# Optimization experiments

Hardware: AMD Instinct MI355X
Metric: run time of the kernel (lower is better)

Reference implementation:

```python
import jax, jax.numpy as jnp
import numpy as np
from jax import lax

N, D, H = 4096, 256, 4


def setup_inputs() -> dict:
    key = jax.random.key(0)
    ks = jax.random.split(key, 6)
    x = jax.random.normal(ks[0], (1, 1, N, D), dtype=jnp.float32)
    adj = jax.random.randint(ks[1], (N, N), 0, 2, dtype=jnp.int32)
    conv_w = jax.random.normal(ks[2], (1, 1, 1, 1), dtype=jnp.float32)
    conv_b = jax.random.normal(ks[3], (1,), dtype=jnp.float32)
    # xavier_uniform on (H, 2D, 1) with gain 1.414
    limit = 1.414 * np.sqrt(6.0 / (2 * D + 1))
    a = jax.random.uniform(ks[4], (H, 2 * D, 1), minval=-limit, maxval=limit, dtype=jnp.float32)
    bias = jnp.zeros((D,), dtype=jnp.float32)
    return {"x": x, "adj": adj, "conv_w": conv_w, "conv_b": conv_b, "a": a, "bias": bias}


def reference(x, adj, conv_w, conv_b, a, bias):
    # 1x1 conv (NCHW / OIHW), preserves spatial dims
    h = lax.conv_general_dilated(x, conv_w, (1, 1), 'VALID',
                                 dimension_numbers=('NCHW', 'OIHW', 'NCHW'))
    h = h + conv_b[None, :, None, None]
    h = h[0, 0]                      # [N, D]
    d = h.shape[1]
    a1 = a[:, :d, 0]                 # [H, D]
    a2 = a[:, d:, 0]                 # [H, D]
    Wh1 = h @ a1.T                   # [N, H]
    Wh2 = h @ a2.T                   # [N, H]
    # e[k, i, j] = elu(Wh1[i, k] + Wh2[j, k])
    e = jax.nn.elu(Wh1.T[:, :, None] + Wh2.T[:, None, :])   # [H, N, N]
    att = jnp.where((adj > 0)[None, :, :], e, jnp.float32(-9e15))
    att = jax.nn.softmax(att, axis=-1)
    # dropout is inactive in eval mode (self.training=False)
    h_pass = jnp.einsum('hij,jd->hid', att, h).mean(axis=0)  # [N, D]
    out = jax.nn.elu(0.5 * h_pass + 0.5 * h)
    norm = jnp.maximum(jnp.linalg.norm(out, axis=1, keepdims=True), 1e-12)
    out = out / norm
    return out + bias
```

## Files before the change

### kernel.cpp

```cpp
#include <hip/hip_runtime.h>
#include <math.h>

#define NN 4096
#define DD 256
#define HH 4
#define SPLIT 8
#define BKG 64

typedef short short8 __attribute__((ext_vector_type(8)));
typedef float float4v __attribute__((ext_vector_type(4)));

__device__ __forceinline__ unsigned short f2bf(float f) {
  unsigned u = __float_as_uint(f);
  u += 0x7FFF + ((u >> 16) & 1);
  return (unsigned short)(u >> 16);
}
__device__ __forceinline__ unsigned f2bf_pk(float a, float b) {
  unsigned ua = __float_as_uint(a); ua += 0x7FFF + ((ua >> 16) & 1);
  unsigned ub = __float_as_uint(b); ub += 0x7FFF + ((ub >> 16) & 1);
  return __builtin_amdgcn_perm(ub, ua, 0x07060302);
}
__device__ __forceinline__ void gld16(void* lds, const void* gp) {
  __builtin_amdgcn_global_load_lds(
      (const __attribute__((address_space(1))) unsigned int*)gp,
      (__attribute__((address_space(3))) unsigned int*)lds, 16, 0, 0);
}

__global__ void k_zero(float* __restrict__ hp) {
  int idx = blockIdx.x * 256 + threadIdx.x;
  ((float4*)hp)[idx] = make_float4(0.f, 0.f, 0.f, 0.f);
}

__global__ __launch_bounds__(256) void k_pre(
    const float* __restrict__ x, const float* __restrict__ a,
    const float* __restrict__ cwp, const float* __restrict__ cbp,
    unsigned short* __restrict__ hbfT, float* __restrict__ Rpg,
    unsigned short* __restrict__ Ebf) {
  const int tid = threadIdx.x;
  const int bid = blockIdx.x;
  const float cw = cwp[0], cb = cbp[0];

  if (bid < 256) {
    __shared__ float t[64][65];
    const int j0 = (bid & 63) * 64, d0 = (bid >> 6) * 64;
    const int r = tid >> 4, c4 = tid & 15;
#pragma unroll
    for (int p = 0; p < 4; p++) {
      const int jj = p * 16 + r;
      const float4 v = *(const float4*)(x + (size_t)(j0 + jj) * DD + d0 + c4 * 4);
      t[jj][c4 * 4 + 0] = v.x * cw + cb;
      t[jj][c4 * 4 + 1] = v.y * cw + cb;
      t[jj][c4 * 4 + 2] = v.z * cw + cb;
      t[jj][c4 * 4 + 3] = v.w * cw + cb;
    }
    __syncthreads();
    const int jc = (tid & 15) * 4, db = tid >> 4;
#pragma unroll
    for (int p = 0; p < 4; p++) {
      const int dd = p * 16 + db;
      const unsigned l0 = f2bf(t[jc + 0][dd]);
      const unsigned l1 = f2bf(t[jc + 1][dd]);
      const unsigned l2 = f2bf(t[jc + 2][dd]);
      const unsigned l3 = f2bf(t[jc + 3][dd]);
      uint2 val;
      val.x = l0 | (l1 << 16);
      val.y = l2 | (l3 << 16);
      *(uint2*)(hbfT + (size_t)(d0 + dd) * NN + j0 + jc) = val;
    }
  } else {
    const int ln = tid >> 2, qd = (tid & 3) * 64;
    const int node = (bid - 256) * 64 + ln;
    float p1[HH] = {0.f, 0.f, 0.f, 0.f}, p2[HH] = {0.f, 0.f, 0.f, 0.f};
#pragma unroll
    for (int k = 0; k < 16; k++) {
      const int d = qd + k * 4;
      const float4 v = *(const float4*)(x + (size_t)node * DD + d);
      const float h0 = v.x * cw + cb, h1 = v.y * cw + cb;
      const float h2 = v.z * cw + cb, h3 = v.w * cw + cb;
#pragma unroll
      for (int h = 0; h < HH; h++) {
        const float4 a1 = *(const float4*)(a + h * 512 + d);
        const float4 a2 = *(const float4*)(a + h * 512 + 256 + d);
        p1[h] += h0 * a1.x + h1 * a1.y + h2 * a1.z + h3 * a1.w;
        p2[h] += h0 * a2.x + h1 * a2.y + h2 * a2.z + h3 * a2.w;
      }
    }
#pragma unroll
    for (int off = 1; off <= 2; off <<= 1) {
#pragma unroll
      for (int h = 0; h < HH; h++) {
        p1[h] += __shfl_xor(p1[h], off);
        p2[h] += __shfl_xor(p2[h], off);
      }
    }
    if ((tid & 3) == 0) {
#pragma unroll
      for (int h = 0; h < HH; h++) {
        Rpg[h * NN + node] = __expf(p1[h]);
        Ebf[h * NN + node] = f2bf(__expf(p2[h]));
      }
    }
  }
}

__global__ __launch_bounds__(256) void k_zw(
    const int* __restrict__ adj, const float* __restrict__ Rpg,
    const unsigned short* __restrict__ Ebf, unsigned short* __restrict__ Wm) {
  __shared__ float red[4][HH];
  __shared__ float sZi[HH];

  const int i = blockIdx.x;
  const int tid = threadIdx.x;
  const float C = 0.36787944117144233f;
  float Rp[HH], z[HH];
#pragma unroll
  for (int h = 0; h < HH; h++) {
    Rp[h] = Rpg[h * NN + i];
    z[h] = 0.f;
  }
  unsigned P[4][HH][2];
  const int4* arow = (const int4*)(adj + (size_t)i * NN);
#pragma unroll
  for (int k = 0; k < 4; k++) {
    const int j4 = tid + k * 256;
    const int4 av = arow[j4];
    const bool m0 = av.x > 0, m1 = av.y > 0, m2 = av.z > 0, m3 = av.w > 0;
#pragma unroll
    for (int h = 0; h < HH; h++) {
      const uint2 e2 = *(const uint2*)(Ebf + (size_t)h * NN + j4 * 4);
      const float E0 = __uint_as_float(e2.x << 16);
      const float E1 = __uint_as_float(e2.x & 0xffff0000u);
      const float E2 = __uint_as_float(e2.y << 16);
      const float E3 = __uint_as_float(e2.y & 0xffff0000u);
      float u, p0, p1, p2, p3;
      u = Rp[h] * E0; p0 = u > 1.f ? u : C * __expf(u); p0 = m0 ? p0 : 0.f;
      u = Rp[h] * E1; p1 = u > 1.f ? u : C * __expf(u); p1 = m1 ? p1 : 0.f;
      u = Rp[h] * E2; p2 = u > 1.f ? u : C * __expf(u); p2 = m2 ? p2 : 0.f;
      u = Rp[h] * E3; p3 = u > 1.f ? u : C * __expf(u); p3 = m3 ? p3 : 0.f;
      z[h] += (p0 + p1) + (p2 + p3);
      P[k][h][0] = f2bf_pk(p0, p1);
      P[k][h][1] = f2bf_pk(p2, p3);
    }
  }
#pragma unroll
  for (int h = 0; h < HH; h++) {
#pragma unroll
    for (int off = 32; off; off >>= 1) z[h] += __shfl_xor(z[h], off);
  }
  const int lane = tid & 63, wv = tid >> 6;
  if (lane == 0) {
#pragma unroll
    for (int h = 0; h < HH; h++) red[wv][h] = z[h];
  }
  __syncthreads();
  if (tid < HH) {
    const float zt = red[0][tid] + red[1][tid] + red[2][tid] + red[3][tid];
    sZi[tid] = zt > 0.f ? 0.25f / zt : 0.f;
  }
  __syncthreads();
  float Zi[HH];
#pragma unroll
  for (int h = 0; h < HH; h++) Zi[h] = sZi[h];

  unsigned* wrow = (unsigned*)(Wm + (size_t)i * NN);
#pragma unroll
  for (int k = 0; k < 4; k++) {
    const int j4 = tid + k * 256;
    float w0 = 0.f, w1 = 0.f, w2 = 0.f, w3 = 0.f;
#pragma unroll
    for (int h = 0; h < HH; h++) {
      const unsigned pa = P[k][h][0];
      const unsigned pb = P[k][h][1];
      w0 += __uint_as_float(pa << 16) * Zi[h];
      w1 += __uint_as_float(pa & 0xffff0000u) * Zi[h];
      w2 += __uint_as_float(pb << 16) * Zi[h];
      w3 += __uint_as_float(pb & 0xffff0000u) * Zi[h];
    }
    wrow[j4 * 2] = f2bf_pk(w0, w1);
    wrow[j4 * 2 + 1] = f2bf_pk(w2, w3);
  }
}

__global__ __launch_bounds__(256) void k_gemm(
    const unsigned short* __restrict__ Wm, const unsigned short* __restrict__ hbfT,
    float* __restrict__ hpOut, int useSplit) {
  __shared__ __align__(16) unsigned short sA[64 * 64];
  __shared__ __align__(16) unsigned short sB[256 * 64];
  const int tid = threadIdx.x;
  const int wv = tid >> 6, lane = tid & 63;
  const int m16 = lane & 15, q = lane >> 4, m7 = m16 & 7;
  const int rb = blockIdx.x >> 3, sp = blockIdx.x & 7;
  const int i0 = rb * 64;
  const int jlo = sp * (NN / SPLIT);
  const int lr = lane >> 3;
  const int lk8 = (lane & 7) ^ lr;

  float4v acc[4][4];
#pragma unroll
  for (int a = 0; a < 4; a++)
#pragma unroll
    for (int b = 0; b < 4; b++) acc[a][b] = (float4v)0.f;

  for (int kt = 0; kt < (NN / SPLIT) / BKG; kt++) {
    const int j0 = jlo + kt * BKG;
    __syncthreads();
#pragma unroll
    for (int t = 0; t < 2; t++) {
      const int r0 = wv * 16 + t * 8;
      gld16(sA + r0 * 64, Wm + (size_t)(i0 + r0 + lr) * NN + j0 + lk8 * 8);
    }
#pragma unroll
    for (int t = 0; t < 8; t++) {
      const int r0 = wv * 64 + t * 8;
      gld16(sB + r0 * 64, hbfT + (size_t)(r0 + lr) * NN + j0 + lk8 * 8);
    }
    __syncthreads();
#pragma unroll
    for (int ks = 0; ks < 2; ks++) {
      const int kp = ((ks * 4 + q) ^ m7) * 8;
      short8 aF[4], bF[4];
#pragma unroll
      for (int it = 0; it < 4; it++)
        aF[it] = *(const short8*)(sA + (it * 16 + m16) * 64 + kp);
#pragma unroll
      for (int dt = 0; dt < 4; dt++)
        bF[dt] = *(const short8*)(sB + (wv * 64 + dt * 16 + m16) * 64 + kp);
#pragma unroll
      for (int it = 0; it < 4; it++)
#pragma unroll
        for (int dt = 0; dt < 4; dt++)
          acc[it][dt] = __builtin_amdgcn_mfma_f32_16x16x32_bf16(aF[it], bF[dt], acc[it][dt], 0, 0, 0);
    }
  }

  if (useSplit) {
    float* base = hpOut + (size_t)sp * NN * DD;
#pragma unroll
    for (int it = 0; it < 4; it++)
#pragma unroll
      for (int dt = 0; dt < 4; dt++) {
        const int d = wv * 64 + dt * 16 + m16;
#pragma unroll
        for (int rg = 0; rg < 4; rg++)
          base[(size_t)(i0 + it * 16 + q * 4 + rg) * DD + d] = acc[it][dt][rg];
      }
  } else {
#pragma unroll
    for (int it = 0; it < 4; it++)
#pragma unroll
      for (int dt = 0; dt < 4; dt++) {
        const int d = wv * 64 + dt * 16 + m16;
#pragma unroll
        for (int rg = 0; rg < 4; rg++)
          atomicAdd(&hpOut[(size_t)(i0 + it * 16 + q * 4 + rg) * DD + d], acc[it][dt][rg]);
      }
  }
}

__global__ __launch_bounds__(256) void k_epi(
    const float* __restrict__ hp, int nsplit, const float* __restrict__ x,
    const float* __restrict__ cwp, const float* __restrict__ cbp,
    const float* __restrict__ bias, float* __restrict__ out) {
  const int lane = threadIdx.x & 63, wv = threadIdx.x >> 6;
  const int i = blockIdx.x * 4 + wv;
  const float cw = cwp[0], cb = cbp[0];
  const int d4 = lane * 4;
  float4 pv = make_float4(0.f, 0.f, 0.f, 0.f);
  for (int s = 0; s < nsplit; s++) {
    const float4 t = *(const float4*)(hp + (size_t)s * NN * DD + (size_t)i * DD + d4);
    pv.x += t.x; pv.y += t.y; pv.z += t.z; pv.w += t.w;
  }
  const float4 xv = *(const float4*)(x + (size_t)i * DD + d4);
  float4 v;
  v.x = 0.5f * pv.x + 0.5f * (xv.x * cw + cb);
  v.y = 0.5f * pv.y + 0.5f * (xv.y * cw + cb);
  v.z = 0.5f * pv.z + 0.5f * (xv.z * cw + cb);
  v.w = 0.5f * pv.w + 0.5f * (xv.w * cw + cb);
  v.x = v.x > 0.f ? v.x : expm1f(v.x);
  v.y = v.y > 0.f ? v.y : expm1f(v.y);
  v.z = v.z > 0.f ? v.z : expm1f(v.z);
  v.w = v.w > 0.f ? v.w : expm1f(v.w);
  float ss = v.x * v.x + v.y * v.y + v.z * v.z + v.w * v.w;
#pragma unroll
  for (int off = 32; off; off >>= 1) ss += __shfl_xor(ss, off);
  const float inv = 1.f / fmaxf(sqrtf(ss), 1e-12f);
  const float4 bv = *(const float4*)(bias + d4);
  float4 o;
  o.x = v.x * inv + bv.x;
  o.y = v.y * inv + bv.y;
  o.z = v.z * inv + bv.z;
  o.w = v.w * inv + bv.w;
  *(float4*)(out + (size_t)i * DD + d4) = o;
}

extern "C" void kernel_launch(void* const* d_in, const int* in_sizes, int n_in,
                              void* d_out, int out_size, void* d_ws, size_t ws_size,
                              hipStream_t stream) {
  const float* x = (const float*)d_in[0];
  const int* adj = (const int*)d_in[1];
  const float* cw = (const float*)d_in[2];
  const float* cb = (const float*)d_in[3];
  const float* a = (const float*)d_in[4];
  const float* bias = (const float*)d_in[5];
  float* out = (float*)d_out;
  float* ws = (float*)d_ws;

  float* Rpg = ws;
  unsigned short* Ebf = (unsigned short*)(ws + 16384);
  unsigned short* hbfT = (unsigned short*)(ws + 24576);
  unsigned short* Wm = (unsigned short*)(ws + 24576 + 524288);
  float* hp = ws + 24576 + 524288 + 8388608;

  const size_t needSplit =
      (size_t)(24576 + 524288 + 8388608 + (size_t)SPLIT * NN * DD) * 4;
  const int useSplit = (ws_size >= needSplit) ? 1 : 0;
  const int nsplit = useSplit ? SPLIT : 1;

  if (!useSplit) hipLaunchKernelGGL(k_zero, dim3(1024), dim3(256), 0, stream, hp);
  hipLaunchKernelGGL(k_pre, dim3(320), dim3(256), 0, stream, x, a, cw, cb, hbfT, Rpg, Ebf);
  hipLaunchKernelGGL(k_zw, dim3(NN), dim3(256), 0, stream, adj, Rpg, Ebf, Wm);
  hipLaunchKernelGGL(k_gemm, dim3(64 * SPLIT), dim3(256), 0, stream, Wm, hbfT, hp, useSplit);
  hipLaunchKernelGGL(k_epi, dim3(1024), dim3(256), 0, stream, hp, nsplit, x, cw, cb, bias, out);
}
```

Before: 165.5 us.

## Double-buffer GEMM LDS tiles and keep attention probabilities in fp32 registers

The GEMM kernel now uses two dynamic shared-memory buffers and issues the global-to-LDS loads for the next K tile before computing on the current one. This removes one barrier per iteration and overlaps load latency with the MFMA work. In exchange, LDS use doubles to 80KB, which can lower occupancy. Separately, k_zw keeps the per-head probabilities as fp32 instead of packing them to bf16. This drops the pack and unpack ALU work and rounding, at the cost of more registers.

```diff
diff --git a/kernel.cpp b/kernel.cpp
--- a/kernel.cpp
+++ b/kernel.cpp
@@ -118,7 +118,7 @@
     Rp[h] = Rpg[h * NN + i];
     z[h] = 0.f;
   }
-  unsigned P[4][HH][2];
+  float P[4][HH][4];
   const int4* arow = (const int4*)(adj + (size_t)i * NN);
 #pragma unroll
   for (int k = 0; k < 4; k++) {
@@ -138,8 +138,7 @@
       u = Rp[h] * E2; p2 = u > 1.f ? u : C * __expf(u); p2 = m2 ? p2 : 0.f;
       u = Rp[h] * E3; p3 = u > 1.f ? u : C * __expf(u); p3 = m3 ? p3 : 0.f;
       z[h] += (p0 + p1) + (p2 + p3);
-      P[k][h][0] = f2bf_pk(p0, p1);
-      P[k][h][1] = f2bf_pk(p2, p3);
+      P[k][h][0] = p0; P[k][h][1] = p1; P[k][h][2] = p2; P[k][h][3] = p3;
     }
   }
 #pragma unroll
@@ -169,12 +168,10 @@
     float w0 = 0.f, w1 = 0.f, w2 = 0.f, w3 = 0.f;
 #pragma unroll
     for (int h = 0; h < HH; h++) {
-      const unsigned pa = P[k][h][0];
-      const unsigned pb = P[k][h][1];
-      w0 += __uint_as_float(pa << 16) * Zi[h];
-      w1 += __uint_as_float(pa & 0xffff0000u) * Zi[h];
-      w2 += __uint_as_float(pb << 16) * Zi[h];
-      w3 += __uint_as_float(pb & 0xffff0000u) * Zi[h];
+      w0 += P[k][h][0] * Zi[h];
+      w1 += P[k][h][1] * Zi[h];
+      w2 += P[k][h][2] * Zi[h];
+      w3 += P[k][h][3] * Zi[h];
     }
     wrow[j4 * 2] = f2bf_pk(w0, w1);
     wrow[j4 * 2 + 1] = f2bf_pk(w2, w3);
@@ -184,8 +181,11 @@
 __global__ __launch_bounds__(256) void k_gemm(
     const unsigned short* __restrict__ Wm, const unsigned short* __restrict__ hbfT,
     float* __restrict__ hpOut, int useSplit) {
-  __shared__ __align__(16) unsigned short sA[64 * 64];
-  __shared__ __align__(16) unsigned short sB[256 * 64];
+  extern __shared__ __align__(16) unsigned short smem[];
+  unsigned short* sA0 = smem;
+  unsigned short* sA1 = smem + 4096;
+  unsigned short* sB0 = smem + 8192;
+  unsigned short* sB1 = smem + 8192 + 16384;
   const int tid = threadIdx.x;
   const int wv = tid >> 6, lane = tid & 63;
   const int m16 = lane & 15, q = lane >> 4, m7 = m16 & 7;
@@ -194,6 +194,7 @@
   const int jlo = sp * (NN / SPLIT);
   const int lr = lane >> 3;
   const int lk8 = (lane & 7) ^ lr;
+  const int NT = (NN / SPLIT) / BKG;
 
   float4v acc[4][4];
 #pragma unroll
@@ -201,36 +202,58 @@
 #pragma unroll
     for (int b = 0; b < 4; b++) acc[a][b] = (float4v)0.f;
 
-  for (int kt = 0; kt < (NN / SPLIT) / BKG; kt++) {
-    const int j0 = jlo + kt * BKG;
-    __syncthreads();
+  {
+    const int j0 = jlo;
 #pragma unroll
     for (int t = 0; t < 2; t++) {
       const int r0 = wv * 16 + t * 8;
-      gld16(sA + r0 * 64, Wm + (size_t)(i0 + r0 + lr) * NN + j0 + lk8 * 8);
+      gld16(sA0 + r0 * 64, Wm + (size_t)(i0 + r0 + lr) * NN + j0 + lk8 * 8);
     }
 #pragma unroll
     for (int t = 0; t < 8; t++) {
       const int r0 = wv * 64 + t * 8;
-      gld16(sB + r0 * 64, hbfT + (size_t)(r0 + lr) * NN + j0 + lk8 * 8);
-    }
-    __syncthreads();
+      gld16(sB0 + r0 * 64, hbfT + (size_t)(r0 + lr) * NN + j0 + lk8 * 8);
+    }
+  }
+  __syncthreads();
+
+  for (int kt = 0; kt < NT; kt++) {
+    const unsigned short* sAb = (kt & 1) ? sA1 : sA0;
+    const unsigned short* sBb = (kt & 1) ? sB1 : sB0;
+    unsigned short* sAn = (kt & 1) ? sA0 : sA1;
+    unsigned short* sBn = (kt & 1) ? sB0 : sB1;
+
+    if (kt + 1 < NT) {
+      const int j0 = jlo + (kt + 1) * BKG;
+#pragma unroll
+      for (int t = 0; t < 2; t++) {
+        const int r0 = wv * 16 + t * 8;
+        gld16(sAn + r0 * 64, Wm + (size_t)(i0 + r0 + lr) * NN + j0 + lk8 * 8);
+      }
+#pragma unroll
+      for (int t = 0; t < 8; t++) {
+        const int r0 = wv * 64 + t * 8;
+        gld16(sBn + r0 * 64, hbfT + (size_t)(r0 + lr) * NN + j0 + lk8 * 8);
+      }
+    }
+
 #pragma unroll
     for (int ks = 0; ks < 2; ks++) {
       const int kp = ((ks * 4 + q) ^ m7) * 8;
       short8 aF[4], bF[4];
 #pragma unroll
       for (int it = 0; it < 4; it++)
-        aF[it] = *(const short8*)(sA + (it * 16 + m16) * 64 + kp);
+        aF[it] = *(const short8*)(sAb + (it * 16 + m16) * 64 + kp);
 #pragma unroll
       for (int dt = 0; dt < 4; dt++)
-        bF[dt] = *(const short8*)(sB + (wv * 64 + dt * 16 + m16) * 64 + kp);
+        bF[dt] = *(const short8*)(sBb + (wv * 64 + dt * 16 + m16) * 64 + kp);
 #pragma unroll
       for (int it = 0; it < 4; it++)
 #pragma unroll
         for (int dt = 0; dt < 4; dt++)
           acc[it][dt] = __builtin_amdgcn_mfma_f32_16x16x32_bf16(aF[it], bF[dt], acc[it][dt], 0, 0, 0);
     }
+    __syncthreads();
   }
 
   if (useSplit) {
@@ -316,9 +339,16 @@
   const int useSplit = (ws_size >= needSplit) ? 1 : 0;
   const int nsplit = useSplit ? SPLIT : 1;
 
+  static int smemDone = 0;
+  if (!smemDone) {
+    (void)hipFuncSetAttribute((const void*)k_gemm,
+                              hipFuncAttributeMaxDynamicSharedMemorySize, 81920);
+    smemDone = 1;
+  }
+
   if (!useSplit) hipLaunchKernelGGL(k_zero, dim3(1024), dim3(256), 0, stream, hp);
   hipLaunchKernelGGL(k_pre, dim3(320), dim3(256), 0, stream, x, a, cw, cb, hbfT, Rpg, Ebf);
   hipLaunchKernelGGL(k_zw, dim3(NN), dim3(256), 0, stream, adj, Rpg, Ebf, Wm);
-  hipLaunchKernelGGL(k_gemm, dim3(64 * SPLIT), dim3(256), 0, stream, Wm, hbfT, hp, useSplit);
+  hipLaunchKernelGGL(k_gemm, dim3(64 * SPLIT), dim3(256), 81920, stream, Wm, hbfT, hp, useSplit);
   hipLaunchKernelGGL(k_epi, dim3(1024), dim3(256), 0, stream, hp, nsplit, x, cw, cb, bias, out);
 }
```

Measured after the change: 162.0 us. 2.1% less time.
